# Performance work log

Hardware: AMD Instinct MI355X
Metric: run time of the kernel (lower is better)

## Reference

```python
import jax, jax.numpy as jnp
import numpy as np

N_EMBD = 2048
N_HEAD = 16
NUM_KV_GROUPS = 2
HEAD_DIM = N_EMBD // N_HEAD  # 128
GROUP_SIZE = N_HEAD // NUM_KV_GROUPS  # 8
EPS = 1e-8


def rmsnorm(x, gamma):
    rms = jnp.sqrt(jnp.mean(x * x, axis=-1, keepdims=True) + EPS)
    return x / rms * gamma


def setup_inputs() -> dict:
    key = jax.random.key(0)
    ks = jax.random.split(key, 10)
    s = 0.02
    x = jax.random.normal(ks[0], (2, 2048, N_EMBD), dtype=jnp.float32)
    Wq = jax.random.normal(ks[1], (N_EMBD, N_HEAD * HEAD_DIM), dtype=jnp.float32) * s
    bq = jnp.zeros((N_HEAD * HEAD_DIM,), jnp.float32)
    Wk = jax.random.normal(ks[2], (N_EMBD, NUM_KV_GROUPS * HEAD_DIM), dtype=jnp.float32) * s
    bk = jnp.zeros((NUM_KV_GROUPS * HEAD_DIM,), jnp.float32)
    Wv = jax.random.normal(ks[3], (N_EMBD, NUM_KV_GROUPS * HEAD_DIM), dtype=jnp.float32) * s
    bv = jnp.zeros((NUM_KV_GROUPS * HEAD_DIM,), jnp.float32)
    gamma_q = jnp.ones((HEAD_DIM,), jnp.float32)
    gamma_k = jnp.ones((HEAD_DIM,), jnp.float32)
    Wo = jax.random.normal(ks[4], (N_EMBD, N_EMBD), dtype=jnp.float32) * s
    bo = jnp.zeros((N_EMBD,), jnp.float32)
    return {"x": x, "Wq": Wq, "bq": bq, "Wk": Wk, "bk": bk, "Wv": Wv, "bv": bv,
            "gamma_q": gamma_q, "gamma_k": gamma_k, "Wo": Wo, "bo": bo}


def reference(x, Wq, bq, Wk, bk, Wv, bv, gamma_q, gamma_k, Wo, bo):
    B, S, E = x.shape
    # projections
    q = (x @ Wq + bq).reshape(B, S, N_HEAD, HEAD_DIM).transpose(0, 2, 1, 3)       # (B,H,S,D)
    k = (x @ Wk + bk).reshape(B, S, NUM_KV_GROUPS, HEAD_DIM).transpose(0, 2, 1, 3)  # (B,G,S,D)
    v = (x @ Wv + bv).reshape(B, S, NUM_KV_GROUPS, HEAD_DIM).transpose(0, 2, 1, 3)
    # fused per-head QK RMSNorm
    q = rmsnorm(q, gamma_q)
    k = rmsnorm(k, gamma_k)
    # GQA: broadcast each KV group to its GROUP_SIZE query heads (repeat_interleave on head dim)
    k = jnp.repeat(k, GROUP_SIZE, axis=1)  # (B,H,S,D)
    v = jnp.repeat(v, GROUP_SIZE, axis=1)
    scores = jnp.einsum('bhqd,bhkd->bhqk', q, k)
    causal = jnp.triu(jnp.ones((S, S), dtype=bool), k=1)
    scores = jnp.where(causal, -jnp.inf, scores)
    weights = jax.nn.softmax(scores / np.sqrt(HEAD_DIM).astype(np.float32), axis=-1)
    context = jnp.einsum('bhqk,bhkd->bhqd', weights, v)
    context = context.transpose(0, 2, 1, 3).reshape(B, S, E)
    return context @ Wo + bo
```

## Files before the change

### kernel.cpp

```cpp
#include <hip/hip_runtime.h>
#include <hip/hip_bf16.h>


typedef short  bf16x8 __attribute__((ext_vector_type(8)));
typedef float  f32x4  __attribute__((ext_vector_type(4)));
typedef unsigned short u16x8 __attribute__((ext_vector_type(8)));

static __device__ __forceinline__ unsigned short f2bf(float f) {
    __hip_bfloat16 h = __float2bfloat16(f);
    return *reinterpret_cast<unsigned short*>(&h);
}

static __device__ __forceinline__ void load_lds16(const void* g, void* l) {
    __builtin_amdgcn_global_load_lds(
        (const __attribute__((address_space(1))) void*)g,
        (__attribute__((address_space(3))) void*)l, 16, 0, 0);
}

__global__ __launch_bounds__(256)
void cvt_bf16_k(const float* __restrict__ X, unsigned short* __restrict__ Y, int n8) {
    int i = blockIdx.x * 256 + threadIdx.x;
    if (i >= n8) return;
    float4 a = *(const float4*)(X + (size_t)i * 8);
    float4 b = *(const float4*)(X + (size_t)i * 8 + 4);
    u16x8 o{f2bf(a.x), f2bf(a.y), f2bf(a.z), f2bf(a.w),
            f2bf(b.x), f2bf(b.y), f2bf(b.z), f2bf(b.w)};
    *(u16x8*)(Y + (size_t)i * 8) = o;
}

__global__ __launch_bounds__(256)
void transpose_cvt2(const float* __restrict__ W, unsigned short* __restrict__ Wt,
                    int in_stride, int K) {
    __shared__ float t[32][33];
    int n0 = blockIdx.x * 32, k0 = blockIdx.y * 32;
    int tx = threadIdx.x & 31, ty = threadIdx.x >> 5;
#pragma unroll
    for (int i = 0; i < 32; i += 8)
        t[ty + i][tx] = W[(size_t)(k0 + ty + i) * in_stride + n0 + tx];
    __syncthreads();
#pragma unroll
    for (int i = 0; i < 32; i += 8)
        Wt[(size_t)(n0 + ty + i) * K + k0 + tx] = f2bf(t[tx][ty + i]);
}

__global__ __launch_bounds__(256)
void gemm_lds(const unsigned short* __restrict__ A, const unsigned short* __restrict__ Bt,
              const float* __restrict__ bias, float* __restrict__ Cout,
              int M, int N, int K) {
    __shared__ unsigned short Al[128 * 32];
    __shared__ unsigned short Bl[128 * 32];
    int m0 = blockIdx.y * 128, n0 = blockIdx.x * 128;
    int tid = threadIdx.x, lane = tid & 63, w = tid >> 6;
    int wr = w >> 1, wc = w & 1, lg = lane >> 4, lr = lane & 15;

    f32x4 acc[4][4];
#pragma unroll
    for (int i = 0; i < 4; i++)
#pragma unroll
        for (int j = 0; j < 4; j++) acc[i][j] = f32x4{0.f, 0.f, 0.f, 0.f};

    int srow = w * 16 + (lane >> 2);
    int scol = (lane & 3) * 8;
    const unsigned short* ga = A  + (size_t)(m0 + srow) * K + scol;
    const unsigned short* gb = Bt + (size_t)(n0 + srow) * K + scol;
    unsigned short* la = Al + w * 512;
    unsigned short* lb = Bl + w * 512;

    for (int k0 = 0; k0 < K; k0 += 32) {
        load_lds16(ga + k0,                    la);
        load_lds16(ga + (size_t)64 * K + k0,   la + 2048);
        load_lds16(gb + k0,                    lb);
        load_lds16(gb + (size_t)64 * K + k0,   lb + 2048);
        __syncthreads();
        bf16x8 af[4], bfv[4];
#pragma unroll
        for (int mi = 0; mi < 4; mi++)
            af[mi] = *(const bf16x8*)&Al[(wr * 64 + mi * 16 + lr) * 32 + 8 * lg];
#pragma unroll
        for (int ni = 0; ni < 4; ni++)
            bfv[ni] = *(const bf16x8*)&Bl[(wc * 64 + ni * 16 + lr) * 32 + 8 * lg];
#pragma unroll
        for (int mi = 0; mi < 4; mi++)
#pragma unroll
            for (int ni = 0; ni < 4; ni++)
                acc[mi][ni] = __builtin_amdgcn_mfma_f32_16x16x32_bf16(af[mi], bfv[ni], acc[mi][ni], 0, 0, 0);
        __syncthreads();
    }

#pragma unroll
    for (int mi = 0; mi < 4; mi++)
#pragma unroll
        for (int ni = 0; ni < 4; ni++) {
            int col = n0 + wc * 64 + ni * 16 + lr;
            float bv = bias[col];
#pragma unroll
            for (int r = 0; r < 4; r++) {
                int row = m0 + wr * 64 + mi * 16 + 4 * lg + r;
                Cout[(size_t)row * N + col] = acc[mi][ni][r] + bv;
            }
        }
}

__global__ __launch_bounds__(256)
void rmsnorm_cvt2(const float* __restrict__ C, const float* __restrict__ gamma,
                  unsigned short* __restrict__ Y, int in_stride, int in_off,
                  int cl, int total) {
    int wave = blockIdx.x * 4 + (threadIdx.x >> 6);
    int lane = threadIdx.x & 63;
    if (wave >= total) return;
    int token = wave >> cl, c = wave & ((1 << cl) - 1);
    const float* in = C + (size_t)token * in_stride + in_off + c * 128;
    float2 v = *(const float2*)(in + lane * 2);
    float ss = v.x * v.x + v.y * v.y;
#pragma unroll
    for (int m = 1; m < 64; m <<= 1) ss += __shfl_xor(ss, m);
    float inv = rsqrtf(ss * (1.0f / 128.0f) + 1e-8f);
    float2 gv = *(const float2*)(gamma + lane * 2);
    unsigned short o0 = f2bf(v.x * inv * gv.x);
    unsigned short o1 = f2bf(v.y * inv * gv.y);
    ((unsigned int*)Y)[((size_t)token * (1 << cl) + c) * 64 + lane] =
        (unsigned)o0 | ((unsigned)o1 << 16);
}

__global__ __launch_bounds__(256, 3)
void attn_kernel(const unsigned short* __restrict__ Qb,
                 const unsigned short* __restrict__ Kb,
                 const unsigned short* __restrict__ Vt,
                 unsigned short* __restrict__ Ctx) {
    const int S = 2048;
    int pair = blockIdx.x, h = blockIdx.y, b = blockIdx.z, g = h >> 3;
    int tid = threadIdx.x, lane = tid & 63, w = tid >> 6;
    int lg = lane >> 4, lr = lane & 15;
    size_t tok0 = (size_t)b * S;

    __shared__ unsigned short Kl[64 * 128];
    __shared__ unsigned short Vl[128 * 64];
    __shared__ unsigned short Pl[4][16][72];

    const float cexp = 0.08838834764831845f * 1.4426950408889634f;

    int krow_l = w * 4 + (lane >> 4);
    int kc16   = (lane & 15) ^ (krow_l & 7);
    int vrow_l = w * 8 + (lane >> 3);
    int vc16   = (lane & 7) ^ (vrow_l & 7);

    for (int hf = 0; hf < 2; hf++) {
        int qt = hf ? (31 - pair) : pair;
        int qrow0 = qt * 64 + w * 16;

        bf16x8 qf[4];
#pragma unroll
        for (int ks = 0; ks < 4; ks++)
            qf[ks] = *(const bf16x8*)(Qb + (tok0 + qrow0 + lr) * 2048 + h * 128 + ks * 32 + 8 * lg);

        f32x4 o[8];
#pragma unroll
        for (int t = 0; t < 8; t++) o[t] = f32x4{0.f, 0.f, 0.f, 0.f};
        float mrow[4], lrow[4];
#pragma unroll
        for (int r = 0; r < 4; r++) { mrow[r] = -1e30f; lrow[r] = 0.f; }

        int nkv = qt + 1;
        for (int kvt = 0; kvt < nkv; kvt++) {
            int kv0 = kvt * 64;
            const unsigned short* ksrc = Kb + (tok0 + kv0 + krow_l) * 256 + g * 128 + kc16 * 8;
#pragma unroll
            for (int i = 0; i < 4; i++)
                load_lds16(ksrc + (size_t)i * 16 * 256, Kl + i * 2048 + w * 512);
            const unsigned short* vsrc = Vt + (size_t)(g * 128 + vrow_l) * 4096 + b * S + kv0 + vc16 * 8;
#pragma unroll
            for (int i = 0; i < 4; i++)
                load_lds16(vsrc + (size_t)i * 32 * 4096, Vl + i * 2048 + w * 512);
            __syncthreads();

            f32x4 sacc[4];
#pragma unroll
            for (int c = 0; c < 4; c++) sacc[c] = f32x4{0.f, 0.f, 0.f, 0.f};
            int kswz = (lr & 7) << 3;
#pragma unroll
            for (int c = 0; c < 4; c++) {
                int krow = c * 16 + lr;
#pragma unroll
                for (int ks = 0; ks < 4; ks++) {
                    bf16x8 kfr = *(const bf16x8*)&Kl[krow * 128 + ((ks * 32 + 8 * lg) ^ kswz)];
                    sacc[c] = __builtin_amdgcn_mfma_f32_16x16x32_bf16(qf[ks], kfr, sacc[c], 0, 0, 0);
                }
            }

            bool diag = (kvt == qt);
            float p[4][4], tmax[4];
#pragma unroll
            for (int r = 0; r < 4; r++) tmax[r] = -1e30f;
#pragma unroll
            for (int c = 0; c < 4; c++)
#pragma unroll
                for (int r = 0; r < 4; r++) {
                    float s = sacc[c][r] * cexp;
                    if (diag) {
                        int qi = qrow0 + 4 * lg + r;
                        int ki = kv0 + c * 16 + lr;
                        if (ki > qi) s = -1e30f;
                    }
                    p[c][r] = s;
                    tmax[r] = fmaxf(tmax[r], s);
                }
#pragma unroll
            for (int m = 1; m < 16; m <<= 1)
#pragma unroll
                for (int r = 0; r < 4; r++)
                    tmax[r] = fmaxf(tmax[r], __shfl_xor(tmax[r], m));

            float alpha[4], tsum[4];
#pragma unroll
            for (int r = 0; r < 4; r++) {
                float mn = fmaxf(mrow[r], tmax[r]);
                alpha[r] = __builtin_exp2f(mrow[r] - mn);
                mrow[r] = mn;
                tsum[r] = 0.f;
            }
#pragma unroll
            for (int c = 0; c < 4; c++)
#pragma unroll
                for (int r = 0; r < 4; r++) {
                    float e = __builtin_exp2f(p[c][r] - mrow[r]);
                    p[c][r] = e;
                    tsum[r] += e;
                }
#pragma unroll
            for (int m = 1; m < 16; m <<= 1)
#pragma unroll
                for (int r = 0; r < 4; r++)
                    tsum[r] += __shfl_xor(tsum[r], m);
#pragma unroll
            for (int r = 0; r < 4; r++)
                lrow[r] = lrow[r] * alpha[r] + tsum[r];
#pragma unroll
            for (int t = 0; t < 8; t++)
#pragma unroll
                for (int r = 0; r < 4; r++) o[t][r] *= alpha[r];

#pragma unroll
            for (int c = 0; c < 4; c++)
#pragma unroll
                for (int r = 0; r < 4; r++)
                    Pl[w][4 * lg + r][c * 16 + lr] = f2bf(p[c][r]);

#pragma unroll
            for (int ks = 0; ks < 2; ks++) {
                bf16x8 pf = *(const bf16x8*)&Pl[w][lr][ks * 32 + 8 * lg];
#pragma unroll
                for (int t = 0; t < 8; t++) {
                    int vrow = t * 16 + lr;
                    bf16x8 vf = *(const bf16x8*)&Vl[vrow * 64 + ((ks * 32 + 8 * lg) ^ kswz)];
                    o[t] = __builtin_amdgcn_mfma_f32_16x16x32_bf16(pf, vf, o[t], 0, 0, 0);
                }
            }
            __syncthreads();
        }

#pragma unroll
        for (int r = 0; r < 4; r++) {
            float inv = 1.0f / lrow[r];
            unsigned short* crow = Ctx + (tok0 + qrow0 + 4 * lg + r) * 2048 + h * 128;
#pragma unroll
            for (int t = 0; t < 8; t++)
                crow[t * 16 + lr] = f2bf(o[t][r] * inv);
        }
    }
}

extern "C" void kernel_launch(void* const* d_in, const int* in_sizes, int n_in,
                              void* d_out, int out_size, void* d_ws, size_t ws_size,
                              hipStream_t stream) {
    const float* x  = (const float*)d_in[0];
    const float* Wq = (const float*)d_in[1];
    const float* bq = (const float*)d_in[2];
    const float* Wk = (const float*)d_in[3];
    const float* bk = (const float*)d_in[4];
    const float* Wv = (const float*)d_in[5];
    const float* bv = (const float*)d_in[6];
    const float* gq = (const float*)d_in[7];
    const float* gk = (const float*)d_in[8];
    const float* Wo = (const float*)d_in[9];
    const float* bo = (const float*)d_in[10];
    float* out = (float*)d_out;

    char* ws = (char*)d_ws;
    size_t off = 0;
    auto alloc = [&](size_t bytes) {
        void* p = ws + off;
        off += (bytes + 255) & ~(size_t)255;
        return p;
    };
    unsigned short* wqkvt = (unsigned short*)alloc((size_t)2560 * 2048 * 2);
    unsigned short* wot   = (unsigned short*)alloc((size_t)2048 * 2048 * 2);
    unsigned short* xb    = (unsigned short*)alloc((size_t)4096 * 2048 * 2);
    float*          C     = (float*)alloc((size_t)4096 * 2560 * 4);
    unsigned short* qb_   = (unsigned short*)alloc((size_t)4096 * 2048 * 2);
    unsigned short* kb_   = (unsigned short*)alloc((size_t)4096 * 256 * 2);
    unsigned short* vt    = (unsigned short*)alloc((size_t)512 * 4096 * 2);
    float*          biascat = (float*)alloc((size_t)2560 * 4);
    unsigned short* ctx = xb;

    cvt_bf16_k<<<4096, 256, 0, stream>>>(x, xb, 1048576);
    transpose_cvt2<<<dim3(64, 64), 256, 0, stream>>>(Wq, wqkvt, 2048, 2048);
    transpose_cvt2<<<dim3(8, 64),  256, 0, stream>>>(Wk, wqkvt + (size_t)2048 * 2048, 256, 2048);
    transpose_cvt2<<<dim3(8, 64),  256, 0, stream>>>(Wv, wqkvt + (size_t)2304 * 2048, 256, 2048);
    transpose_cvt2<<<dim3(64, 64), 256, 0, stream>>>(Wo, wot, 2048, 2048);
    hipMemcpyAsync(biascat,        bq, 2048 * 4, hipMemcpyDeviceToDevice, stream);
    hipMemcpyAsync(biascat + 2048, bk,  256 * 4, hipMemcpyDeviceToDevice, stream);
    hipMemcpyAsync(biascat + 2304, bv,  256 * 4, hipMemcpyDeviceToDevice, stream);

    gemm_lds<<<dim3(20, 32), 256, 0, stream>>>(xb, wqkvt, biascat, C, 4096, 2560, 2048);

    rmsnorm_cvt2<<<16384, 256, 0, stream>>>(C, gq, qb_, 2560, 0,    4, 65536);
    rmsnorm_cvt2<<<2048,  256, 0, stream>>>(C, gk, kb_, 2560, 2048, 1, 8192);
    transpose_cvt2<<<dim3(16, 128), 256, 0, stream>>>(C + 2304, vt, 2560, 4096);

    attn_kernel<<<dim3(16, 16, 2), 256, 0, stream>>>(qb_, kb_, vt, ctx);

    gemm_lds<<<dim3(16, 32), 256, 0, stream>>>(ctx, wot, bo, out, 4096, 2048, 2048);
}
```

Measured before the change: 373.8 us.

## Double-buffer GEMM, swizzle workgroups, and fuse two query tiles per attention block

The GEMM now double-buffers its LDS tiles so the next K-slice loads while the current one computes, and remaps workgroup IDs with an XCD-aware swizzle. The attention kernel handles both causal-paired query tiles in a single KV sweep, so each K/V fragment is fetched once for both tiles. K and V now go straight from global memory into registers instead of through LDS, which removes the per-tile barriers. It also computes transposed scores, skips the online-softmax rescale unless the running max grows by more than a threshold, and stages outputs through LDS for vector stores. The three bias memcpys become a single concat kernel; the trade-offs are higher register pressure (occupancy hint drops from 3 to 2) and more global and L2 traffic for K/V.

```diff
diff --git a/kernel.cpp b/kernel.cpp
--- a/kernel.cpp
+++ b/kernel.cpp
@@ -44,12 +44,24 @@
 }
 
 __global__ __launch_bounds__(256)
+void concat_bias(const float* __restrict__ bq, const float* __restrict__ bk,
+                 const float* __restrict__ bv, float* __restrict__ o) {
+    int i = blockIdx.x * 256 + threadIdx.x;
+    if (i >= 2560) return;
+    o[i] = (i < 2048) ? bq[i] : (i < 2304 ? bk[i - 2048] : bv[i - 2304]);
+}
+
+__global__ __launch_bounds__(256)
 void gemm_lds(const unsigned short* __restrict__ A, const unsigned short* __restrict__ Bt,
               const float* __restrict__ bias, float* __restrict__ Cout,
               int M, int N, int K) {
-    __shared__ unsigned short Al[128 * 32];
-    __shared__ unsigned short Bl[128 * 32];
-    int m0 = blockIdx.y * 128, n0 = blockIdx.x * 128;
+    __shared__ unsigned short Al[2][128 * 32];
+    __shared__ unsigned short Bl[2][128 * 32];
+    int nwg = gridDim.x * gridDim.y;
+    int bid = blockIdx.y * gridDim.x + blockIdx.x;
+    int swz = (bid & 7) * (nwg >> 3) + (bid >> 3);
+    int m0 = (swz / gridDim.x) * 128, n0 = (swz % gridDim.x) * 128;
+
     int tid = threadIdx.x, lane = tid & 63, w = tid >> 6;
     int wr = w >> 1, wc = w & 1, lg = lane >> 4, lr = lane & 15;
 
@@ -63,22 +75,28 @@
     int scol = (lane & 3) * 8;
     const unsigned short* ga = A  + (size_t)(m0 + srow) * K + scol;
     const unsigned short* gb = Bt + (size_t)(n0 + srow) * K + scol;
-    unsigned short* la = Al + w * 512;
-    unsigned short* lb = Bl + w * 512;
+
+    auto stage = [&](int buf, int k0) {
+        unsigned short* la = &Al[buf][w * 512];
+        unsigned short* lb = &Bl[buf][w * 512];
+        load_lds16(ga + k0,                  la);
+        load_lds16(ga + (size_t)64 * K + k0, la + 2048);
+        load_lds16(gb + k0,                  lb);
+        load_lds16(gb + (size_t)64 * K + k0, lb + 2048);
+    };
+    stage(0, 0);
+    __syncthreads();
 
     for (int k0 = 0; k0 < K; k0 += 32) {
-        load_lds16(ga + k0,                    la);
-        load_lds16(ga + (size_t)64 * K + k0,   la + 2048);
-        load_lds16(gb + k0,                    lb);
-        load_lds16(gb + (size_t)64 * K + k0,   lb + 2048);
-        __syncthreads();
+        int cur = (k0 >> 5) & 1;
+        if (k0 + 32 < K) stage(cur ^ 1, k0 + 32);
         bf16x8 af[4], bfv[4];
 #pragma unroll
         for (int mi = 0; mi < 4; mi++)
-            af[mi] = *(const bf16x8*)&Al[(wr * 64 + mi * 16 + lr) * 32 + 8 * lg];
+            af[mi] = *(const bf16x8*)&Al[cur][(wr * 64 + mi * 16 + lr) * 32 + 8 * lg];
 #pragma unroll
         for (int ni = 0; ni < 4; ni++)
-            bfv[ni] = *(const bf16x8*)&Bl[(wc * 64 + ni * 16 + lr) * 32 + 8 * lg];
+            bfv[ni] = *(const bf16x8*)&Bl[cur][(wc * 64 + ni * 16 + lr) * 32 + 8 * lg];
 #pragma unroll
         for (int mi = 0; mi < 4; mi++)
 #pragma unroll
@@ -122,151 +140,155 @@
         (unsigned)o0 | ((unsigned)o1 << 16);
 }
 
-__global__ __launch_bounds__(256, 3)
+__global__ __launch_bounds__(256, 2)
 void attn_kernel(const unsigned short* __restrict__ Qb,
                  const unsigned short* __restrict__ Kb,
                  const unsigned short* __restrict__ Vt,
                  unsigned short* __restrict__ Ctx) {
     const int S = 2048;
-    int pair = blockIdx.x, h = blockIdx.y, b = blockIdx.z, g = h >> 3;
+    int bid = blockIdx.x;
+    int xcd = bid & 7, ii = bid >> 3;
+    int g2 = xcd >> 1;
+    int local = (xcd & 1) * 64 + ii;
+    int pair = local & 15, hl = local >> 4;
+    int b = g2 >> 1, g = g2 & 1, h = g * 8 + hl;
+
     int tid = threadIdx.x, lane = tid & 63, w = tid >> 6;
     int lg = lane >> 4, lr = lane & 15;
     size_t tok0 = (size_t)b * S;
 
-    __shared__ unsigned short Kl[64 * 128];
-    __shared__ unsigned short Vl[128 * 64];
-    __shared__ unsigned short Pl[4][16][72];
+    int qtA = pair, qtB = 31 - pair;
+    int qA0 = qtA * 64 + w * 16, qB0 = qtB * 64 + w * 16;
+
+    __shared__ unsigned short Pl[4][2][16][72];
+    __shared__ unsigned short Ob[4][16][136];
 
     const float cexp = 0.08838834764831845f * 1.4426950408889634f;
 
-    int krow_l = w * 4 + (lane >> 4);
-    int kc16   = (lane & 15) ^ (krow_l & 7);
-    int vrow_l = w * 8 + (lane >> 3);
-    int vc16   = (lane & 7) ^ (vrow_l & 7);
-
-    for (int hf = 0; hf < 2; hf++) {
-        int qt = hf ? (31 - pair) : pair;
-        int qrow0 = qt * 64 + w * 16;
-
-        bf16x8 qf[4];
-#pragma unroll
-        for (int ks = 0; ks < 4; ks++)
-            qf[ks] = *(const bf16x8*)(Qb + (tok0 + qrow0 + lr) * 2048 + h * 128 + ks * 32 + 8 * lg);
-
-        f32x4 o[8];
-#pragma unroll
-        for (int t = 0; t < 8; t++) o[t] = f32x4{0.f, 0.f, 0.f, 0.f};
-        float mrow[4], lrow[4];
-#pragma unroll
-        for (int r = 0; r < 4; r++) { mrow[r] = -1e30f; lrow[r] = 0.f; }
-
-        int nkv = qt + 1;
-        for (int kvt = 0; kvt < nkv; kvt++) {
-            int kv0 = kvt * 64;
-            const unsigned short* ksrc = Kb + (tok0 + kv0 + krow_l) * 256 + g * 128 + kc16 * 8;
-#pragma unroll
-            for (int i = 0; i < 4; i++)
-                load_lds16(ksrc + (size_t)i * 16 * 256, Kl + i * 2048 + w * 512);
-            const unsigned short* vsrc = Vt + (size_t)(g * 128 + vrow_l) * 4096 + b * S + kv0 + vc16 * 8;
-#pragma unroll
-            for (int i = 0; i < 4; i++)
-                load_lds16(vsrc + (size_t)i * 32 * 4096, Vl + i * 2048 + w * 512);
-            __syncthreads();
-
-            f32x4 sacc[4];
-#pragma unroll
-            for (int c = 0; c < 4; c++) sacc[c] = f32x4{0.f, 0.f, 0.f, 0.f};
-            int kswz = (lr & 7) << 3;
-#pragma unroll
-            for (int c = 0; c < 4; c++) {
-                int krow = c * 16 + lr;
-#pragma unroll
-                for (int ks = 0; ks < 4; ks++) {
-                    bf16x8 kfr = *(const bf16x8*)&Kl[krow * 128 + ((ks * 32 + 8 * lg) ^ kswz)];
-                    sacc[c] = __builtin_amdgcn_mfma_f32_16x16x32_bf16(qf[ks], kfr, sacc[c], 0, 0, 0);
-                }
-            }
-
-            bool diag = (kvt == qt);
-            float p[4][4], tmax[4];
-#pragma unroll
-            for (int r = 0; r < 4; r++) tmax[r] = -1e30f;
+    bf16x8 qfA[4], qfB[4];
+#pragma unroll
+    for (int ks = 0; ks < 4; ks++) {
+        qfA[ks] = *(const bf16x8*)(Qb + (tok0 + qA0 + lr) * 2048 + h * 128 + ks * 32 + 8 * lg);
+        qfB[ks] = *(const bf16x8*)(Qb + (tok0 + qB0 + lr) * 2048 + h * 128 + ks * 32 + 8 * lg);
+    }
+
+    f32x4 oA[8], oB[8];
+#pragma unroll
+    for (int t = 0; t < 8; t++) { oA[t] = f32x4{0.f,0.f,0.f,0.f}; oB[t] = f32x4{0.f,0.f,0.f,0.f}; }
+    float mA = -1e30f, lA = 0.f, mB = -1e30f, lB = 0.f;
+
+    const unsigned short* kb0 = Kb + tok0 * 256 + g * 128 + 8 * lg;
+    const unsigned short* vb0 = Vt + ((size_t)(g * 128 + lr)) * 4096 + tok0 + 8 * lg;
+
+    for (int kvt = 0; kvt <= qtB; kvt++) {
+        int kv0 = kvt * 64;
+        bool doA = (kvt <= qtA);
+
+        f32x4 sA[4], sB[4];
+#pragma unroll
+        for (int c = 0; c < 4; c++) { sA[c] = f32x4{0.f,0.f,0.f,0.f}; sB[c] = f32x4{0.f,0.f,0.f,0.f}; }
+#pragma unroll
+        for (int c = 0; c < 4; c++) {
+            bf16x8 kf[4];
+#pragma unroll
+            for (int ks = 0; ks < 4; ks++)
+                kf[ks] = *(const bf16x8*)(kb0 + (size_t)(kv0 + c * 16 + lr) * 256 + ks * 32);
+#pragma unroll
+            for (int ks = 0; ks < 4; ks++) {
+                sB[c] = __builtin_amdgcn_mfma_f32_16x16x32_bf16(kf[ks], qfB[ks], sB[c], 0, 0, 0);
+                if (doA)
+                    sA[c] = __builtin_amdgcn_mfma_f32_16x16x32_bf16(kf[ks], qfA[ks], sA[c], 0, 0, 0);
+            }
+        }
+
+        auto softmax_half = [&](f32x4 (&sacc)[4], float& mX, float& lX, f32x4 (&oX)[8],
+                                int qX0, bool diagtile, int pslot) {
+            float pv[4][4];
+            float pm = -1e30f;
 #pragma unroll
             for (int c = 0; c < 4; c++)
 #pragma unroll
                 for (int r = 0; r < 4; r++) {
                     float s = sacc[c][r] * cexp;
-                    if (diag) {
-                        int qi = qrow0 + 4 * lg + r;
-                        int ki = kv0 + c * 16 + lr;
-                        if (ki > qi) s = -1e30f;
-                    }
-                    p[c][r] = s;
-                    tmax[r] = fmaxf(tmax[r], s);
+                    if (diagtile && (kv0 + 16 * c + 4 * lg + r > qX0 + lr)) s = -1e30f;
+                    pv[c][r] = s;
+                    pm = fmaxf(pm, s);
                 }
-#pragma unroll
-            for (int m = 1; m < 16; m <<= 1)
-#pragma unroll
-                for (int r = 0; r < 4; r++)
-                    tmax[r] = fmaxf(tmax[r], __shfl_xor(tmax[r], m));
-
-            float alpha[4], tsum[4];
-#pragma unroll
-            for (int r = 0; r < 4; r++) {
-                float mn = fmaxf(mrow[r], tmax[r]);
-                alpha[r] = __builtin_exp2f(mrow[r] - mn);
-                mrow[r] = mn;
-                tsum[r] = 0.f;
-            }
+            pm = fmaxf(pm, __shfl_xor(pm, 16));
+            pm = fmaxf(pm, __shfl_xor(pm, 32));
+            if (!__all(pm <= mX + 8.0f)) {
+                float mn = fmaxf(mX, pm);
+                float al = __builtin_exp2f(mX - mn);
+                mX = mn;
+                lX *= al;
+#pragma unroll
+                for (int t = 0; t < 8; t++)
+#pragma unroll
+                    for (int r = 0; r < 4; r++) oX[t][r] *= al;
+            }
+            float ts = 0.f;
 #pragma unroll
             for (int c = 0; c < 4; c++)
 #pragma unroll
                 for (int r = 0; r < 4; r++) {
-                    float e = __builtin_exp2f(p[c][r] - mrow[r]);
-                    p[c][r] = e;
-                    tsum[r] += e;
+                    float e = __builtin_exp2f(pv[c][r] - mX);
+                    pv[c][r] = e;
+                    ts += e;
                 }
-#pragma unroll
-            for (int m = 1; m < 16; m <<= 1)
-#pragma unroll
-                for (int r = 0; r < 4; r++)
-                    tsum[r] += __shfl_xor(tsum[r], m);
-#pragma unroll
-            for (int r = 0; r < 4; r++)
-                lrow[r] = lrow[r] * alpha[r] + tsum[r];
-#pragma unroll
-            for (int t = 0; t < 8; t++)
-#pragma unroll
-                for (int r = 0; r < 4; r++) o[t][r] *= alpha[r];
-
+            ts += __shfl_xor(ts, 16);
+            ts += __shfl_xor(ts, 32);
+            lX += ts;
 #pragma unroll
             for (int c = 0; c < 4; c++)
 #pragma unroll
-                for (int r = 0; r < 4; r++)
-                    Pl[w][4 * lg + r][c * 16 + lr] = f2bf(p[c][r]);
-
-#pragma unroll
-            for (int ks = 0; ks < 2; ks++) {
-                bf16x8 pf = *(const bf16x8*)&Pl[w][lr][ks * 32 + 8 * lg];
-#pragma unroll
-                for (int t = 0; t < 8; t++) {
-                    int vrow = t * 16 + lr;
-                    bf16x8 vf = *(const bf16x8*)&Vl[vrow * 64 + ((ks * 32 + 8 * lg) ^ kswz)];
-                    o[t] = __builtin_amdgcn_mfma_f32_16x16x32_bf16(pf, vf, o[t], 0, 0, 0);
+                for (int e = 0; e < 2; e++) {
+                    unsigned u = (unsigned)f2bf(pv[c][2 * e]) |
+                                 ((unsigned)f2bf(pv[c][2 * e + 1]) << 16);
+                    *(unsigned*)&Pl[w][pslot][lr][16 * c + 4 * lg + 2 * e] = u;
                 }
-            }
-            __syncthreads();
-        }
-
-#pragma unroll
-        for (int r = 0; r < 4; r++) {
-            float inv = 1.0f / lrow[r];
-            unsigned short* crow = Ctx + (tok0 + qrow0 + 4 * lg + r) * 2048 + h * 128;
-#pragma unroll
-            for (int t = 0; t < 8; t++)
-                crow[t * 16 + lr] = f2bf(o[t][r] * inv);
+        };
+        softmax_half(sB, mB, lB, oB, qB0, kvt == qtB, 0);
+        if (doA) softmax_half(sA, mA, lA, oA, qA0, kvt == qtA, 1);
+
+        bf16x8 pB0 = *(const bf16x8*)&Pl[w][0][lr][8 * lg];
+        bf16x8 pB1 = *(const bf16x8*)&Pl[w][0][lr][32 + 8 * lg];
+        bf16x8 pA0, pA1;
+        if (doA) {
+            pA0 = *(const bf16x8*)&Pl[w][1][lr][8 * lg];
+            pA1 = *(const bf16x8*)&Pl[w][1][lr][32 + 8 * lg];
+        }
+#pragma unroll
+        for (int t = 0; t < 8; t++) {
+            bf16x8 v0 = *(const bf16x8*)(vb0 + (size_t)t * 16 * 4096 + kv0);
+            bf16x8 v1 = *(const bf16x8*)(vb0 + (size_t)t * 16 * 4096 + kv0 + 32);
+            oB[t] = __builtin_amdgcn_mfma_f32_16x16x32_bf16(v0, pB0, oB[t], 0, 0, 0);
+            oB[t] = __builtin_amdgcn_mfma_f32_16x16x32_bf16(v1, pB1, oB[t], 0, 0, 0);
+            if (doA) {
+                oA[t] = __builtin_amdgcn_mfma_f32_16x16x32_bf16(v0, pA0, oA[t], 0, 0, 0);
+                oA[t] = __builtin_amdgcn_mfma_f32_16x16x32_bf16(v1, pA1, oA[t], 0, 0, 0);
+            }
         }
     }
+
+    auto epilogue = [&](f32x4 (&oX)[8], float lX, int qX0) {
+        float inv = 1.0f / lX;
+#pragma unroll
+        for (int t = 0; t < 8; t++)
+#pragma unroll
+            for (int e = 0; e < 2; e++) {
+                unsigned u = (unsigned)f2bf(oX[t][2 * e] * inv) |
+                             ((unsigned)f2bf(oX[t][2 * e + 1] * inv) << 16);
+                *(unsigned*)&Ob[w][lr][16 * t + 4 * lg + 2 * e] = u;
+            }
+        int orow = lane >> 2, oc = lane & 3;
+#pragma unroll
+        for (int p = 0; p < 4; p++) {
+            bf16x8 vv = *(const bf16x8*)&Ob[w][orow][(oc + 4 * p) * 8];
+            *(bf16x8*)(Ctx + (tok0 + qX0 + orow) * 2048 + h * 128 + (oc + 4 * p) * 8) = vv;
+        }
+    };
+    epilogue(oB, lB, qB0);
+    epilogue(oA, lA, qA0);
 }
 
 extern "C" void kernel_launch(void* const* d_in, const int* in_sizes, int n_in,
@@ -307,9 +329,7 @@
     transpose_cvt2<<<dim3(8, 64),  256, 0, stream>>>(Wk, wqkvt + (size_t)2048 * 2048, 256, 2048);
     transpose_cvt2<<<dim3(8, 64),  256, 0, stream>>>(Wv, wqkvt + (size_t)2304 * 2048, 256, 2048);
     transpose_cvt2<<<dim3(64, 64), 256, 0, stream>>>(Wo, wot, 2048, 2048);
-    hipMemcpyAsync(biascat,        bq, 2048 * 4, hipMemcpyDeviceToDevice, stream);
-    hipMemcpyAsync(biascat + 2048, bk,  256 * 4, hipMemcpyDeviceToDevice, stream);
-    hipMemcpyAsync(biascat + 2304, bv,  256 * 4, hipMemcpyDeviceToDevice, stream);
+    concat_bias<<<10, 256, 0, stream>>>(bq, bk, bv, biascat);
 
     gemm_lds<<<dim3(20, 32), 256, 0, stream>>>(xb, wqkvt, biascat, C, 4096, 2560, 2048);
 
@@ -317,7 +337,7 @@
     rmsnorm_cvt2<<<2048,  256, 0, stream>>>(C, gk, kb_, 2560, 2048, 1, 8192);
     transpose_cvt2<<<dim3(16, 128), 256, 0, stream>>>(C + 2304, vt, 2560, 4096);
 
-    attn_kernel<<<dim3(16, 16, 2), 256, 0, stream>>>(qb_, kb_, vt, ctx);
+    attn_kernel<<<512, 256, 0, stream>>>(qb_, kb_, vt, ctx);
 
     gemm_lds<<<dim3(16, 32), 256, 0, stream>>>(ctx, wot, bo, out, 4096, 2048, 2048);
 }
```

Measured after the change: 1.191 ms. 219% more time.
